# Optimization experiments

Measured on AMD Instinct MI355X. Metric: run time of the kernel, lower is better.

Reference implementation:

```python
import jax, jax.numpy as jnp
import numpy as np

NUM_TOKENS = 1024
HIDDEN = 2048
INTER = 4096
EXPERTS = 8


def setup_inputs() -> dict:
    key = jax.random.key(0)
    k1, k2, k3 = jax.random.split(key, 3)
    permuted_tokens = jax.random.normal(k1, (NUM_TOKENS, HIDDEN), dtype=jnp.float32)
    # equal split of tokens across experts (tokens are pre-sorted by expert)
    tokens_per_expert = jnp.full((EXPERTS,), NUM_TOKENS // EXPERTS, dtype=jnp.int32)
    w1 = jax.random.normal(k2, (EXPERTS, HIDDEN, 2 * INTER), dtype=jnp.float32) * (HIDDEN ** -0.5)
    w2 = jax.random.normal(k3, (EXPERTS, INTER, HIDDEN), dtype=jnp.float32) * (INTER ** -0.5)
    return {"permuted_tokens": permuted_tokens, "w1": w1, "w2": w2,
            "tokens_per_expert": tokens_per_expert}


def _grouped_gemm(x, weights, tokens_per_expert):
    # x: [N, K], weights: [E, K, M], tokens sorted by expert with counts tokens_per_expert.
    n = x.shape[0]
    num_experts = weights.shape[0]
    bounds = jnp.cumsum(tokens_per_expert)                      # [E]
    expert_id = jnp.searchsorted(bounds, jnp.arange(n), side='right')  # [N]
    onehot = jax.nn.one_hot(expert_id, num_experts, dtype=x.dtype)     # [N, E]
    out = jnp.zeros((n, weights.shape[-1]), dtype=x.dtype)
    for e in range(num_experts):  # small fixed expert count
        out = out + (x * onehot[:, e:e + 1]) @ weights[e]
    return out


def reference(permuted_tokens, w1, w2, tokens_per_expert):
    fc1 = _grouped_gemm(permuted_tokens, w1, tokens_per_expert)   # [N, 2*I]
    projection, gate = jnp.split(fc1, 2, axis=-1)
    hidden = jax.nn.silu(projection) * gate                        # [N, I]
    return _grouped_gemm(hidden, w2, tokens_per_expert)            # [N, H]
```

## Files before the change

kernel.cpp:

```cpp
#include <hip/hip_runtime.h>

typedef __bf16 bf16;
typedef __attribute__((ext_vector_type(8))) __bf16 bf16x8;
typedef __attribute__((ext_vector_type(4))) __bf16 bf16x4;
typedef __attribute__((ext_vector_type(4))) float floatx4;

#define MFMA16(a, b, c) __builtin_amdgcn_mfma_f32_16x16x32_bf16((a), (b), (c), 0, 0, 0)

constexpr int NTOK = 1024;
constexpr int HID  = 2048;
constexpr int INTER = 4096;
constexpr int TPE  = 128;


__global__ __launch_bounds__(256) void kconvx(const float* __restrict__ x,
                                              bf16* __restrict__ xsw) {
  int gid  = blockIdx.x * 256 + threadIdx.x;
  int w    = gid >> 6;
  int lane = gid & 63;
  int R = w >> 6;
  int T = w & 63;
  int m  = R * 16 + (lane & 15);
  int k0 = T * 32 + ((lane >> 4) << 3);
  const float4* s = reinterpret_cast<const float4*>(x + (size_t)m * HID + k0);
  float4 f0 = s[0], f1 = s[1];
  bf16x8 v;
  v[0] = (bf16)f0.x; v[1] = (bf16)f0.y; v[2] = (bf16)f0.z; v[3] = (bf16)f0.w;
  v[4] = (bf16)f1.x; v[5] = (bf16)f1.y; v[6] = (bf16)f1.z; v[7] = (bf16)f1.w;
  *reinterpret_cast<bf16x8*>(xsw + ((size_t)(R * 64 + T) * 512 + lane * 8)) = v;
}

__global__ __launch_bounds__(256, 2) void kfc1(const bf16* __restrict__ xsw,
                                               const float* __restrict__ w1,
                                               bf16* __restrict__ hid) {
  __shared__ __align__(16) bf16 Ws[128 * 40];
  __shared__ __align__(16) bf16 Hs[4 * 32 * 72];

  const int b = blockIdx.x, e = b >> 6, cb = b & 63;
  const int t = threadIdx.x, lane = t & 63, wv = t >> 6;
  constexpr int WROW = 2 * INTER;

  const float* w1e = w1 + (size_t)e * HID * WROW;
  const int ln = t & 127;
  const int lk = (t >> 7) << 4;
  const int ncol = (ln < 64) ? (cb * 64 + ln) : (INTER + cb * 64 + (ln - 64));
  const float* pk = w1e + (size_t)lk * WROW + ncol;

  floatx4 acc[2][8];
#pragma unroll
  for (int a = 0; a < 2; a++)
#pragma unroll
    for (int n = 0; n < 8; n++) acc[a][n] = (floatx4){0.f, 0.f, 0.f, 0.f};

  float wc[16], wn[16];
#pragma unroll
  for (int i = 0; i < 16; i++) wc[i] = pk[i * WROW];
  pk += 32 * WROW;

  const int boff = (lane & 15) * 40 + ((lane >> 4) << 3);
  const size_t abase0 = (size_t)((e * 8 + wv * 2) * 64) * 512 + lane * 8;
  const size_t abase1 = abase0 + (size_t)64 * 512;

  for (int ks = 0; ks < 64; ks++) {
    bf16x8 wlo, whi;
#pragma unroll
    for (int i = 0; i < 8; i++) { wlo[i] = (bf16)wc[i]; whi[i] = (bf16)wc[8 + i]; }
    __syncthreads();
    *reinterpret_cast<bf16x8*>(&Ws[ln * 40 + lk])     = wlo;
    *reinterpret_cast<bf16x8*>(&Ws[ln * 40 + lk + 8]) = whi;
    if (ks < 63) {
#pragma unroll
      for (int i = 0; i < 16; i++) wn[i] = pk[i * WROW];
      pk += 32 * WROW;
    }
    bf16x8 a0 = *reinterpret_cast<const bf16x8*>(xsw + abase0 + (size_t)ks * 512);
    bf16x8 a1 = *reinterpret_cast<const bf16x8*>(xsw + abase1 + (size_t)ks * 512);
    __syncthreads();
#pragma unroll
    for (int nt = 0; nt < 8; nt++) {
      bf16x8 bfr = *reinterpret_cast<const bf16x8*>(&Ws[nt * 16 * 40 + boff]);
      acc[0][nt] = MFMA16(a0, bfr, acc[0][nt]);
      acc[1][nt] = MFMA16(a1, bfr, acc[1][nt]);
    }
#pragma unroll
    for (int i = 0; i < 16; i++) wc[i] = wn[i];
  }

  bf16* He = &Hs[wv * 32 * 72];
  const int q = lane >> 4, li = lane & 15;
#pragma unroll
  for (int mt = 0; mt < 2; mt++)
#pragma unroll
    for (int nt = 0; nt < 4; nt++)
#pragma unroll
      for (int r = 0; r < 4; r++) {
        float p = acc[mt][nt][r], g = acc[mt][nt + 4][r];
        float hv = p / (1.f + __expf(-p)) * g;
        He[(mt * 16 + q * 4 + r) * 72 + nt * 16 + li] = (bf16)hv;
      }
  __syncthreads();
#pragma unroll
  for (int rb = 0; rb < 2; rb++)
#pragma unroll
    for (int tb = 0; tb < 2; tb++) {
      bf16x8 hv = *reinterpret_cast<const bf16x8*>(
          &He[(rb * 16 + li) * 72 + tb * 32 + (q << 3)]);
      size_t Rg = (size_t)(e * 8 + wv * 2 + rb);
      size_t Tg = (size_t)(cb * 2 + tb);
      *reinterpret_cast<bf16x8*>(hid + (Rg * 128 + Tg) * 512 + lane * 8) = hv;
    }
}

__global__ __launch_bounds__(256, 2) void kfc2(const bf16* __restrict__ hid,
                                               const float* __restrict__ w2,
                                               float* __restrict__ out) {
  __shared__ __align__(16) bf16 Ws[32 * 40];

  const int b = blockIdx.x, e = b >> 6, nb = b & 63, c0 = nb * 32;
  const int t = threadIdx.x, lane = t & 63, wv = t >> 6;

  const float* w2e = w2 + (size_t)e * INTER * HID;
  const int ln = t & 31;
  const int lk4 = (t >> 5) << 2;
  const float* pk = w2e + (size_t)lk4 * HID + (c0 + ln);

  floatx4 acc[2][2];
#pragma unroll
  for (int a = 0; a < 2; a++)
#pragma unroll
    for (int n = 0; n < 2; n++) acc[a][n] = (floatx4){0.f, 0.f, 0.f, 0.f};

  float wc[4], wn[4];
#pragma unroll
  for (int i = 0; i < 4; i++) wc[i] = pk[i * HID];
  pk += 32 * HID;

  const int boff = (lane & 15) * 40 + ((lane >> 4) << 3);
  const size_t abase0 = (size_t)((e * 8 + wv * 2) * 128) * 512 + lane * 8;
  const size_t abase1 = abase0 + (size_t)128 * 512;

  for (int ks = 0; ks < 128; ks++) {
    bf16x4 wl;
#pragma unroll
    for (int i = 0; i < 4; i++) wl[i] = (bf16)wc[i];
    __syncthreads();
    *reinterpret_cast<bf16x4*>(&Ws[ln * 40 + lk4]) = wl;
    if (ks < 127) {
#pragma unroll
      for (int i = 0; i < 4; i++) wn[i] = pk[i * HID];
      pk += 32 * HID;
    }
    bf16x8 a0 = *reinterpret_cast<const bf16x8*>(hid + abase0 + (size_t)ks * 512);
    bf16x8 a1 = *reinterpret_cast<const bf16x8*>(hid + abase1 + (size_t)ks * 512);
    __syncthreads();
#pragma unroll
    for (int nt = 0; nt < 2; nt++) {
      bf16x8 bfr = *reinterpret_cast<const bf16x8*>(&Ws[nt * 16 * 40 + boff]);
      acc[0][nt] = MFMA16(a0, bfr, acc[0][nt]);
      acc[1][nt] = MFMA16(a1, bfr, acc[1][nt]);
    }
#pragma unroll
    for (int i = 0; i < 4; i++) wc[i] = wn[i];
  }

  const int q = lane >> 4, li = lane & 15;
#pragma unroll
  for (int mt = 0; mt < 2; mt++)
#pragma unroll
    for (int nt = 0; nt < 2; nt++)
#pragma unroll
      for (int r = 0; r < 4; r++) {
        int row = e * TPE + wv * 32 + mt * 16 + q * 4 + r;
        int col = c0 + nt * 16 + li;
        out[(size_t)row * HID + col] = acc[mt][nt][r];
      }
}

extern "C" void kernel_launch(void* const* d_in, const int* in_sizes, int n_in,
                              void* d_out, int out_size, void* d_ws, size_t ws_size,
                              hipStream_t stream) {
  const float* x  = (const float*)d_in[0];
  const float* w1 = (const float*)d_in[1];
  const float* w2 = (const float*)d_in[2];
  float* out = (float*)d_out;

  bf16* xsw = (bf16*)d_ws;
  bf16* hid = (bf16*)((char*)d_ws + (size_t)NTOK * HID * 2);

  kconvx<<<(NTOK / 16) * (HID / 32) / 4, 256, 0, stream>>>(x, xsw);
  kfc1<<<8 * (INTER / 64), 256, 0, stream>>>(xsw, w1, hid);
  kfc2<<<8 * (HID / 32), 256, 0, stream>>>(hid, w2, out);
}
```

Before: 882.7 us.

## Vectorize weight loads to float4 and double-buffer LDS in both FFN GEMMs

Weight tiles are now read as float4 along the output columns rather than as scalar strided loads, then transposed into LDS as bf16 pairs. The shared weight tile is double-buffered, so each k-step needs one barrier instead of two. The fc2 kernel also doubles its k-step to 64 so there are fewer iterations and barriers. In exchange it uses more LDS and writes to LDS with smaller stores that may cause bank conflicts.

```diff
diff --git a/kernel.cpp b/kernel.cpp
--- a/kernel.cpp
+++ b/kernel.cpp
@@ -2,7 +2,7 @@
 
 typedef __bf16 bf16;
 typedef __attribute__((ext_vector_type(8))) __bf16 bf16x8;
-typedef __attribute__((ext_vector_type(4))) __bf16 bf16x4;
+typedef __attribute__((ext_vector_type(2))) __bf16 bf16x2;
 typedef __attribute__((ext_vector_type(4))) float floatx4;
 
 #define MFMA16(a, b, c) __builtin_amdgcn_mfma_f32_16x16x32_bf16((a), (b), (c), 0, 0, 0)
@@ -33,7 +33,7 @@
 __global__ __launch_bounds__(256, 2) void kfc1(const bf16* __restrict__ xsw,
                                                const float* __restrict__ w1,
                                                bf16* __restrict__ hid) {
-  __shared__ __align__(16) bf16 Ws[128 * 40];
+  __shared__ __align__(16) bf16 Ws[2][128 * 40];
   __shared__ __align__(16) bf16 Hs[4 * 32 * 72];
 
   const int b = blockIdx.x, e = b >> 6, cb = b & 63;
@@ -41,49 +41,59 @@
   constexpr int WROW = 2 * INTER;
 
   const float* w1e = w1 + (size_t)e * HID * WROW;
-  const int ln = t & 127;
-  const int lk = (t >> 7) << 4;
-  const int ncol = (ln < 64) ? (cb * 64 + ln) : (INTER + cb * 64 + (ln - 64));
-  const float* pk = w1e + (size_t)lk * WROW + ncol;
+  const int kp = t >> 4;
+  const int c4 = (t & 15) * 4;
+  const float* pg = w1e + (size_t)(2 * kp) * WROW + cb * 64 + c4;
+
+  float4 gp0, gp1, gg0, gg1;
+  auto LOADW = [&]() {
+    gp0 = *reinterpret_cast<const float4*>(pg);
+    gp1 = *reinterpret_cast<const float4*>(pg + WROW);
+    gg0 = *reinterpret_cast<const float4*>(pg + INTER);
+    gg1 = *reinterpret_cast<const float4*>(pg + WROW + INTER);
+    pg += (size_t)32 * WROW;
+  };
+  auto STOREW = [&](bf16* wsb) {
+    bf16* base = wsb + c4 * 40 + 2 * kp;
+    const float* a0 = (const float*)&gp0; const float* a1 = (const float*)&gp1;
+    const float* b0 = (const float*)&gg0; const float* b1 = (const float*)&gg1;
+#pragma unroll
+    for (int i = 0; i < 4; i++) {
+      bf16x2 vp, vg;
+      vp[0] = (bf16)a0[i]; vp[1] = (bf16)a1[i];
+      vg[0] = (bf16)b0[i]; vg[1] = (bf16)b1[i];
+      *reinterpret_cast<bf16x2*>(base + i * 40)        = vp;
+      *reinterpret_cast<bf16x2*>(base + (64 + i) * 40) = vg;
+    }
+  };
 
   floatx4 acc[2][8];
 #pragma unroll
   for (int a = 0; a < 2; a++)
 #pragma unroll
     for (int n = 0; n < 8; n++) acc[a][n] = (floatx4){0.f, 0.f, 0.f, 0.f};
-
-  float wc[16], wn[16];
-#pragma unroll
-  for (int i = 0; i < 16; i++) wc[i] = pk[i * WROW];
-  pk += 32 * WROW;
 
   const int boff = (lane & 15) * 40 + ((lane >> 4) << 3);
   const size_t abase0 = (size_t)((e * 8 + wv * 2) * 64) * 512 + lane * 8;
   const size_t abase1 = abase0 + (size_t)64 * 512;
 
+  LOADW();
+  STOREW(Ws[0]);
+  __syncthreads();
+
   for (int ks = 0; ks < 64; ks++) {
-    bf16x8 wlo, whi;
-#pragma unroll
-    for (int i = 0; i < 8; i++) { wlo[i] = (bf16)wc[i]; whi[i] = (bf16)wc[8 + i]; }
-    __syncthreads();
-    *reinterpret_cast<bf16x8*>(&Ws[ln * 40 + lk])     = wlo;
-    *reinterpret_cast<bf16x8*>(&Ws[ln * 40 + lk + 8]) = whi;
-    if (ks < 63) {
-#pragma unroll
-      for (int i = 0; i < 16; i++) wn[i] = pk[i * WROW];
-      pk += 32 * WROW;
-    }
+    if (ks < 63) LOADW();
     bf16x8 a0 = *reinterpret_cast<const bf16x8*>(xsw + abase0 + (size_t)ks * 512);
     bf16x8 a1 = *reinterpret_cast<const bf16x8*>(xsw + abase1 + (size_t)ks * 512);
-    __syncthreads();
+    const bf16* cur = Ws[ks & 1];
 #pragma unroll
     for (int nt = 0; nt < 8; nt++) {
-      bf16x8 bfr = *reinterpret_cast<const bf16x8*>(&Ws[nt * 16 * 40 + boff]);
+      bf16x8 bfr = *reinterpret_cast<const bf16x8*>(cur + nt * 640 + boff);
       acc[0][nt] = MFMA16(a0, bfr, acc[0][nt]);
       acc[1][nt] = MFMA16(a1, bfr, acc[1][nt]);
     }
-#pragma unroll
-    for (int i = 0; i < 16; i++) wc[i] = wn[i];
+    if (ks < 63) STOREW(Ws[(ks + 1) & 1]);
+    __syncthreads();
   }
 
   bf16* He = &Hs[wv * 32 * 72];
@@ -114,15 +124,32 @@
 __global__ __launch_bounds__(256, 2) void kfc2(const bf16* __restrict__ hid,
                                                const float* __restrict__ w2,
                                                float* __restrict__ out) {
-  __shared__ __align__(16) bf16 Ws[32 * 40];
+  __shared__ __align__(16) bf16 Ws[2][32 * 72];
 
   const int b = blockIdx.x, e = b >> 6, nb = b & 63, c0 = nb * 32;
   const int t = threadIdx.x, lane = t & 63, wv = t >> 6;
 
   const float* w2e = w2 + (size_t)e * INTER * HID;
-  const int ln = t & 31;
-  const int lk4 = (t >> 5) << 2;
-  const float* pk = w2e + (size_t)lk4 * HID + (c0 + ln);
+  const int kp = t >> 3;
+  const int c4 = (t & 7) * 4;
+  const float* pg = w2e + (size_t)(2 * kp) * HID + c0 + c4;
+
+  float4 g0, g1;
+  auto LOADW = [&]() {
+    g0 = *reinterpret_cast<const float4*>(pg);
+    g1 = *reinterpret_cast<const float4*>(pg + HID);
+    pg += (size_t)64 * HID;
+  };
+  auto STOREW = [&](bf16* wsb) {
+    bf16* base = wsb + c4 * 72 + 2 * kp;
+    const float* a0 = (const float*)&g0; const float* a1 = (const float*)&g1;
+#pragma unroll
+    for (int i = 0; i < 4; i++) {
+      bf16x2 v;
+      v[0] = (bf16)a0[i]; v[1] = (bf16)a1[i];
+      *reinterpret_cast<bf16x2*>(base + i * 72) = v;
+    }
+  };
 
   floatx4 acc[2][2];
 #pragma unroll
@@ -130,37 +157,30 @@
 #pragma unroll
     for (int n = 0; n < 2; n++) acc[a][n] = (floatx4){0.f, 0.f, 0.f, 0.f};
 
-  float wc[4], wn[4];
-#pragma unroll
-  for (int i = 0; i < 4; i++) wc[i] = pk[i * HID];
-  pk += 32 * HID;
-
-  const int boff = (lane & 15) * 40 + ((lane >> 4) << 3);
+  const int boff = (lane & 15) * 72 + ((lane >> 4) << 3);
   const size_t abase0 = (size_t)((e * 8 + wv * 2) * 128) * 512 + lane * 8;
   const size_t abase1 = abase0 + (size_t)128 * 512;
 
-  for (int ks = 0; ks < 128; ks++) {
-    bf16x4 wl;
-#pragma unroll
-    for (int i = 0; i < 4; i++) wl[i] = (bf16)wc[i];
+  LOADW();
+  STOREW(Ws[0]);
+  __syncthreads();
+
+  for (int ks = 0; ks < 64; ks++) {
+    if (ks < 63) LOADW();
+    const bf16* cur = Ws[ks & 1];
+#pragma unroll
+    for (int ksub = 0; ksub < 2; ksub++) {
+      bf16x8 a0 = *reinterpret_cast<const bf16x8*>(hid + abase0 + (size_t)(ks * 2 + ksub) * 512);
+      bf16x8 a1 = *reinterpret_cast<const bf16x8*>(hid + abase1 + (size_t)(ks * 2 + ksub) * 512);
+      bf16x8 b0 = *reinterpret_cast<const bf16x8*>(cur + boff + ksub * 32);
+      bf16x8 b1 = *reinterpret_cast<const bf16x8*>(cur + 16 * 72 + boff + ksub * 32);
+      acc[0][0] = MFMA16(a0, b0, acc[0][0]);
+      acc[0][1] = MFMA16(a0, b1, acc[0][1]);
+      acc[1][0] = MFMA16(a1, b0, acc[1][0]);
+      acc[1][1] = MFMA16(a1, b1, acc[1][1]);
+    }
+    if (ks < 63) STOREW(Ws[(ks + 1) & 1]);
     __syncthreads();
-    *reinterpret_cast<bf16x4*>(&Ws[ln * 40 + lk4]) = wl;
-    if (ks < 127) {
-#pragma unroll
-      for (int i = 0; i < 4; i++) wn[i] = pk[i * HID];
-      pk += 32 * HID;
-    }
-    bf16x8 a0 = *reinterpret_cast<const bf16x8*>(hid + abase0 + (size_t)ks * 512);
-    bf16x8 a1 = *reinterpret_cast<const bf16x8*>(hid + abase1 + (size_t)ks * 512);
-    __syncthreads();
-#pragma unroll
-    for (int nt = 0; nt < 2; nt++) {
-      bf16x8 bfr = *reinterpret_cast<const bf16x8*>(&Ws[nt * 16 * 40 + boff]);
-      acc[0][nt] = MFMA16(a0, bfr, acc[0][nt]);
-      acc[1][nt] = MFMA16(a1, bfr, acc[1][nt]);
-    }
-#pragma unroll
-    for (int i = 0; i < 4; i++) wc[i] = wn[i];
   }
 
   const int q = lane >> 4, li = lane & 15;
```

New measurement: 873.9 us. No clear change (-1.0%).
